# Optimization experiments

Hardware: AMD Instinct MI355X
Metric: run time of the kernel (lower is better)

Reference implementation:

```python
import jax, jax.numpy as jnp
import numpy as np
from jax import lax

B, T, D_IN = 64, 4096, 64
D_EMB, H = 24, 128


def setup_inputs() -> dict:
    key = jax.random.key(0)
    ks = jax.random.split(key, 8)
    s = 0.01  # matches RandomNormal(stddev=0.01) style init
    return {
        "x": jax.random.normal(ks[0], (B, T, D_IN), jnp.float32),
        "W_emb": jax.random.normal(ks[1], (D_IN, D_EMB), jnp.float32) * s,
        "b_emb": jnp.zeros((D_EMB,), jnp.float32),
        "W_f": jax.random.normal(ks[2], (D_EMB + H, H), jnp.float32) * s,
        "b_f": jnp.ones((H,), jnp.float32),  # forget bias init to ones (as in source)
        "W_i": jax.random.normal(ks[3], (D_EMB + H, H), jnp.float32) * s,
        "b_i": jnp.zeros((H,), jnp.float32),
        "W_c": jax.random.normal(ks[4], (D_EMB + H, H), jnp.float32) * s,
        "b_c": jnp.zeros((H,), jnp.float32),
        "W_o": jax.random.normal(ks[5], (D_EMB + H, H), jnp.float32) * s,
        "b_o": jnp.zeros((H,), jnp.float32),
        "W_out": jax.random.normal(ks[6], (H, 1), jnp.float32) * s,
        "b_out": jnp.zeros((1,), jnp.float32),
    }


def reference(x, W_emb, b_emb, W_f, b_f, W_i, b_i, W_c, b_c, W_o, b_o, W_out, b_out):
    # embedding: Dense(24, sigmoid) applied per timestep
    e = jax.nn.sigmoid(jnp.einsum('btd,de->bte', x, W_emb) + b_emb)  # [B,T,24]
    e_t = jnp.swapaxes(e, 0, 1)  # [T,B,24] for scan over time

    def step(carry, et):
        h, c = carry
        z = jnp.concatenate([et, h], axis=-1)            # [B, 24+128]
        f = jax.nn.sigmoid(z @ W_f + b_f)
        i = jax.nn.sigmoid(z @ W_i + b_i)
        g = jnp.tanh(z @ W_c + b_c)
        o = jax.nn.sigmoid(z @ W_o + b_o)
        c_new = c * f + i * g
        h_new = jnp.tanh(c_new) * o
        return (h_new, c_new), None

    h0 = jnp.zeros((x.shape[0], W_f.shape[1]), x.dtype)
    c0 = jnp.zeros_like(h0)
    (hT, _), _ = lax.scan(step, (h0, c0), e_t)
    return jax.nn.sigmoid(hT @ W_out + b_out)  # [B,1]
```

## Files before the change

kernel.cpp:

```cpp
#include <hip/hip_runtime.h>
#include <stdint.h>

namespace {
constexpr int kB = 64, kT = 4096, kDin = 64, kDe = 24, kH = 128;
constexpr int kCh = 16;
constexpr int kNCh = kT / kCh;
constexpr int kRowU = 16;
constexpr int kPS = 20;
constexpr float kLog2e = 1.4426950408889634f;

typedef __attribute__((ext_vector_type(8))) _Float16 frag8;
typedef __attribute__((ext_vector_type(4))) float v4f;
typedef __attribute__((ext_vector_type(8))) int v8i;
union H2U { uint32_t u; _Float16 s[2]; };

__device__ __forceinline__ float rcp_fast(float x){
#if __has_builtin(__builtin_amdgcn_rcpf)
  return __builtin_amdgcn_rcpf(x);
#else
  return 1.0f / x;
#endif
}
__device__ __forceinline__ float exp2_f(float x){
#if __has_builtin(__builtin_amdgcn_exp2f)
  return __builtin_amdgcn_exp2f(x);
#else
  return exp2f(x);
#endif
}
__device__ __forceinline__ float sigmoid_f(float x){
  return rcp_fast(1.0f + __expf(-x));
}
__device__ __forceinline__ uint32_t pack2(float lo, float hi){
  H2U u; u.s[0] = (_Float16)lo; u.s[1] = (_Float16)hi; return u.u;
}
__device__ __forceinline__ uint32_t sw_fp8(float x){
  union{float f; uint32_t u;} v; v.f = x;
  uint32_t s = (v.u >> 24) & 0x80u;
  float a = fabsf(x);
  if (a < 0.0009765625f) return s;
  if (a > 448.0f) a = 448.0f;
  int e; float m = frexpf(a, &e);
  int E = e - 1 + 7;
  uint32_t bits;
  if (E <= 0){
    int q = (int)(a * 512.0f + 0.5f); if (q > 7) q = 7; bits = (uint32_t)q;
  } else {
    int q = (int)(m * 16.0f + 0.5f);
    if (q == 16){ q = 8; ++E; }
    if (E > 15) { E = 15; q = 14; }
    bits = ((uint32_t)E << 3) | ((uint32_t)q & 7u);
  }
  return s | bits;
}
template <bool HI>
__device__ __forceinline__ uint32_t fp8pair(float a, float b, uint32_t old){
#if __has_builtin(__builtin_amdgcn_cvt_pk_fp8_f32)
  return (uint32_t)__builtin_amdgcn_cvt_pk_fp8_f32(a, b, (int)old, HI);
#else
  uint32_t p = sw_fp8(a) | (sw_fp8(b) << 8);
  return HI ? ((old & 0x0000ffffu) | (p << 16)) : ((old & 0xffff0000u) | p);
#endif
}
__device__ __forceinline__ void lgkm_barrier(){
  asm volatile("s_waitcnt lgkmcnt(0)" ::: "memory");
  __builtin_amdgcn_sched_barrier(0);
  __builtin_amdgcn_s_barrier();
  __builtin_amdgcn_sched_barrier(0);
  asm volatile("" ::: "memory");
}
}

__global__ __launch_bounds__(256) void emb_kernel(
    const float* __restrict__ x, const float* __restrict__ W,
    const float* __restrict__ bias, uint32_t* __restrict__ e_out)
{
  int r = blockIdx.x * blockDim.x + threadIdx.x;
  if (r >= kB * kT) return;
  const float4* xr = (const float4*)(x + (size_t)r * kDin);
  float acc[kDe];
#pragma unroll
  for (int k = 0; k < kDe; ++k) acc[k] = bias[k];
#pragma unroll 4
  for (int d4 = 0; d4 < kDin / 4; ++d4){
    float4 xv = xr[d4];
    const float* w0 = W + (size_t)(d4 * 4) * kDe;
#pragma unroll
    for (int k = 0; k < kDe; ++k) acc[k] += xv.x * w0[k];
#pragma unroll
    for (int k = 0; k < kDe; ++k) acc[k] += xv.y * w0[kDe + k];
#pragma unroll
    for (int k = 0; k < kDe; ++k) acc[k] += xv.z * w0[2 * kDe + k];
#pragma unroll
    for (int k = 0; k < kDe; ++k) acc[k] += xv.w * w0[3 * kDe + k];
  }
  uint32_t p[12];
#pragma unroll
  for (int k = 0; k < 12; ++k)
    p[k] = pack2(sigmoid_f(acc[2 * k]), sigmoid_f(acc[2 * k + 1]));
  uint4* dst = (uint4*)(e_out + (size_t)r * kRowU);
  dst[0] = make_uint4(p[0], p[1], p[2],  p[3]);
  dst[1] = make_uint4(p[4], p[5], p[6],  p[7]);
  dst[2] = make_uint4(p[8], p[9], p[10], p[11]);
  dst[3] = make_uint4(0u, 0u, 0u, 0u);
}

__global__ __launch_bounds__(512, 1) void lstm_kernel(
    const uint32_t* __restrict__ e_ws,
    const float* __restrict__ W_f, const float* __restrict__ b_f,
    const float* __restrict__ W_i, const float* __restrict__ b_i,
    const float* __restrict__ W_c, const float* __restrict__ b_c,
    const float* __restrict__ W_o, const float* __restrict__ b_o,
    const float* __restrict__ W_out, const float* __restrict__ b_out,
    float* __restrict__ out)
{
  __shared__ __align__(16) float preh[4 * kH * kPS];
  __shared__ __align__(16) uint32_t elds[kCh * kRowU];
  __shared__ __align__(64) uint32_t hfp8[2 * 32];
  __shared__ float red[8];

  const int b  = blockIdx.x;
  const int t0 = threadIdx.x;
  const int w  = t0 >> 6;
  const int l  = t0 & 63;
  const int q  = l >> 4;
  const int cl = l & 15;
  const int u  = w * 16 + cl;

  const float* Wg[4] = {W_f, W_i, W_c, W_o};
  const float* bgp[4] = {b_f, b_i, b_c, b_o};
  const float scl[4] = {-kLog2e, -kLog2e, -2.0f * kLog2e, -kLog2e};

  v8i B8[4];
#pragma unroll
  for (int g = 0; g < 4; ++g){
    const float sc = scl[g] * 64.0f;
#pragma unroll
    for (int r = 0; r < 8; ++r){
      const float* col = Wg[g] + (size_t)(24 + q * 32 + r * 4) * kH + u;
      uint32_t reg = fp8pair<false>(col[0] * sc, col[kH] * sc, 0u);
      reg = fp8pair<true>(col[2 * kH] * sc, col[3 * kH] * sc, reg);
      B8[g][r] = (int)reg;
    }
  }

  frag8 Bp[4];
  float biasC[4];
#pragma unroll
  for (int g = 0; g < 4; ++g){
    biasC[g] = bgp[g][u] * scl[g];
#pragma unroll
    for (int j = 0; j < 8; ++j){
      int k = q * 8 + j;
      Bp[g][j] = (_Float16)((k < kDe) ? Wg[g][(size_t)k * kH + u] * scl[g] : 0.0f);
    }
  }

  const uint4* e4 = (const uint4*)e_ws;
  const size_t bbase = (size_t)b * kT * 4;

  auto do_pregemm = [&](){
    frag8 Ae = *(const frag8*)&elds[cl * kRowU + q * 4];
#pragma unroll
    for (int g = 0; g < 4; ++g){
      v4f c; c[0] = biasC[g]; c[1] = biasC[g]; c[2] = biasC[g]; c[3] = biasC[g];
      v4f d = __builtin_amdgcn_mfma_f32_16x16x32_f16(Ae, Bp[g], c, 0, 0, 0);
      *(v4f*)&preh[(g * kH + u) * kPS + q * 4] = d;
    }
  };
  float pb[4][kCh];
  auto load_pb = [&](){
#pragma unroll
    for (int g = 0; g < 4; ++g){
      const v4f* src = (const v4f*)&preh[(g * kH + u) * kPS];
#pragma unroll
      for (int r = 0; r < 4; ++r){
        v4f t = src[r];
        pb[g][4*r+0] = t[0]; pb[g][4*r+1] = t[1];
        pb[g][4*r+2] = t[2]; pb[g][4*r+3] = t[3];
      }
    }
  };

  uint4 pre4;
  if (t0 < 64) ((uint4*)elds)[t0] = e4[bbase + t0];
  if (t0 < 32) hfp8[t0] = 0u;
  __syncthreads();
  do_pregemm();
  load_pb();
  if (t0 < 64 && kNCh > 1) pre4 = e4[bbase + (size_t)kCh * 4 + t0];

  float cst = 0.0f, ho = 0.0f;
  const v4f zero4 = {0.0f, 0.0f, 0.0f, 0.0f};

#pragma unroll 1
  for (int cc = 0; cc < kNCh; ++cc){
#pragma unroll
    for (int s = 0; s < kCh; ++s){
      const int cur = (cc * kCh + s) & 1, nxt = cur ^ 1;

      v8i A = *(const v8i*)&hfp8[cur * 32 + q * 8];

      v4f a0 = __builtin_amdgcn_mfma_scale_f32_16x16x128_f8f6f4(
                   A, B8[0], zero4, 0, 0, 0, 121, 0, 121);
      v4f a1 = __builtin_amdgcn_mfma_scale_f32_16x16x128_f8f6f4(
                   A, B8[1], zero4, 0, 0, 0, 121, 0, 121);
      v4f a2 = __builtin_amdgcn_mfma_scale_f32_16x16x128_f8f6f4(
                   A, B8[2], zero4, 0, 0, 0, 121, 0, 121);
      v4f a3 = __builtin_amdgcn_mfma_scale_f32_16x16x128_f8f6f4(
                   A, B8[3], zero4, 0, 0, 0, 121, 0, 121);

      float f  = rcp_fast(1.0f + exp2_f(a0[0] + pb[0][s]));
      float ig = rcp_fast(1.0f + exp2_f(a1[0] + pb[1][s]));
      float g2 = rcp_fast(1.0f + exp2_f(a2[0] + pb[2][s]));
      float og = rcp_fast(1.0f + exp2_f(a3[0] + pb[3][s]));
      float gg = fmaf(g2, 2.0f, -1.0f);
      cst = fmaf(cst, f, ig * gg);
      float rh = rcp_fast(1.0f + exp2_f(-2.0f * kLog2e * cst));
      ho = fmaf(rh, 128.0f, -64.0f) * og;

      if (l < 16){
        uint32_t byte = fp8pair<false>(ho, ho, 0u) & 0xffu;
        ((uint8_t*)&hfp8[nxt * 32])[u] = (uint8_t)byte;
      }
      if (s == kCh - 1 && cc + 1 < kNCh && t0 < 64) ((uint4*)elds)[t0] = pre4;
      lgkm_barrier();
    }

    if (cc + 1 < kNCh){
      do_pregemm();
      load_pb();
      if (t0 < 64 && cc + 2 < kNCh)
        pre4 = e4[bbase + (size_t)(cc + 2) * kCh * 4 + t0];
    }
  }

  float partial = (l < 16) ? ho * (W_out[u] * 0.015625f) : 0.0f;
#pragma unroll
  for (int off = 1; off <= 32; off <<= 1) partial += __shfl_xor(partial, off, 64);
  if (l == 0) red[w] = partial;
  __syncthreads();
  if (t0 == 0){
    float acc = b_out[0];
#pragma unroll
    for (int k = 0; k < 8; ++k) acc += red[k];
    out[b] = sigmoid_f(acc);
  }
}

extern "C" void kernel_launch(void* const* d_in, const int* in_sizes, int n_in,
                              void* d_out, int out_size, void* d_ws, size_t ws_size,
                              hipStream_t stream){
  const float* x     = (const float*)d_in[0];
  const float* W_emb = (const float*)d_in[1];
  const float* b_emb = (const float*)d_in[2];
  const float* W_f   = (const float*)d_in[3];
  const float* b_f   = (const float*)d_in[4];
  const float* W_i   = (const float*)d_in[5];
  const float* b_i   = (const float*)d_in[6];
  const float* W_c   = (const float*)d_in[7];
  const float* b_c   = (const float*)d_in[8];
  const float* W_o   = (const float*)d_in[9];
  const float* b_o   = (const float*)d_in[10];
  const float* W_out = (const float*)d_in[11];
  const float* b_out = (const float*)d_in[12];
  float* out = (float*)d_out;
  uint32_t* e_ws = (uint32_t*)d_ws;

  const int rows = kB * kT;
  emb_kernel<<<(rows + 255) / 256, 256, 0, stream>>>(x, W_emb, b_emb, e_ws);
  lstm_kernel<<<kB, 512, 0, stream>>>(e_ws, W_f, b_f, W_i, b_i, W_c, b_c,
                                      W_o, b_o, W_out, b_out, out);
}
```

Baseline: 1.444 ms.

## Halve LSTM block to 4 waves, each wave handling two hidden-unit slices

Shrinks the recurrent block from 8 to 4 wavefronts, so each wave computes two 16-unit hidden slices per step with 8 MFMAs instead of 4. The goal is cheaper per-step barrier synchronization across fewer waves on the serial time loop. To fit the doubled per-lane state in registers, the precomputed input-projection terms are stored packed as fp16 pairs rather than fp32, which lowers their precision. Per-wave work per step doubles, so the serial critical path may grow.

```diff
diff --git a/kernel.cpp b/kernel.cpp
--- a/kernel.cpp
+++ b/kernel.cpp
@@ -105,7 +105,7 @@
   dst[3] = make_uint4(0u, 0u, 0u, 0u);
 }
 
-__global__ __launch_bounds__(512, 1) void lstm_kernel(
+__global__ __launch_bounds__(256, 1) void lstm_kernel(
     const uint32_t* __restrict__ e_ws,
     const float* __restrict__ W_f, const float* __restrict__ b_f,
     const float* __restrict__ W_i, const float* __restrict__ b_i,
@@ -117,7 +117,7 @@
   __shared__ __align__(16) float preh[4 * kH * kPS];
   __shared__ __align__(16) uint32_t elds[kCh * kRowU];
   __shared__ __align__(64) uint32_t hfp8[2 * 32];
-  __shared__ float red[8];
+  __shared__ float red[4];
 
   const int b  = blockIdx.x;
   const int t0 = threadIdx.x;
@@ -125,34 +125,41 @@
   const int l  = t0 & 63;
   const int q  = l >> 4;
   const int cl = l & 15;
-  const int u  = w * 16 + cl;
+  const int u  = w * 32 + cl;
 
   const float* Wg[4] = {W_f, W_i, W_c, W_o};
   const float* bgp[4] = {b_f, b_i, b_c, b_o};
   const float scl[4] = {-kLog2e, -kLog2e, -2.0f * kLog2e, -kLog2e};
 
-  v8i B8[4];
-#pragma unroll
-  for (int g = 0; g < 4; ++g){
-    const float sc = scl[g] * 64.0f;
-#pragma unroll
-    for (int r = 0; r < 8; ++r){
-      const float* col = Wg[g] + (size_t)(24 + q * 32 + r * 4) * kH + u;
-      uint32_t reg = fp8pair<false>(col[0] * sc, col[kH] * sc, 0u);
-      reg = fp8pair<true>(col[2 * kH] * sc, col[3 * kH] * sc, reg);
-      B8[g][r] = (int)reg;
-    }
-  }
-
-  frag8 Bp[4];
-  float biasC[4];
-#pragma unroll
-  for (int g = 0; g < 4; ++g){
-    biasC[g] = bgp[g][u] * scl[g];
-#pragma unroll
-    for (int j = 0; j < 8; ++j){
-      int k = q * 8 + j;
-      Bp[g][j] = (_Float16)((k < kDe) ? Wg[g][(size_t)k * kH + u] * scl[g] : 0.0f);
+  v8i B8[2][4];
+#pragma unroll
+  for (int sl = 0; sl < 2; ++sl){
+#pragma unroll
+    for (int g = 0; g < 4; ++g){
+      const float sc = scl[g] * 64.0f;
+#pragma unroll
+      for (int r = 0; r < 8; ++r){
+        const float* col = Wg[g] + (size_t)(24 + q * 32 + r * 4) * kH + (u + sl * 16);
+        uint32_t reg = fp8pair<false>(col[0] * sc, col[kH] * sc, 0u);
+        reg = fp8pair<true>(col[2 * kH] * sc, col[3 * kH] * sc, reg);
+        B8[sl][g][r] = (int)reg;
+      }
+    }
+  }
+
+  frag8 Bp[2][4];
+  float biasC[2][4];
+#pragma unroll
+  for (int sl = 0; sl < 2; ++sl){
+#pragma unroll
+    for (int g = 0; g < 4; ++g){
+      biasC[sl][g] = bgp[g][u + sl * 16] * scl[g];
+#pragma unroll
+      for (int j = 0; j < 8; ++j){
+        int k = q * 8 + j;
+        Bp[sl][g][j] =
+            (_Float16)((k < kDe) ? Wg[g][(size_t)k * kH + (u + sl * 16)] * scl[g] : 0.0f);
+      }
     }
   }
 
@@ -162,35 +169,46 @@
   auto do_pregemm = [&](){
     frag8 Ae = *(const frag8*)&elds[cl * kRowU + q * 4];
 #pragma unroll
-    for (int g = 0; g < 4; ++g){
-      v4f c; c[0] = biasC[g]; c[1] = biasC[g]; c[2] = biasC[g]; c[3] = biasC[g];
-      v4f d = __builtin_amdgcn_mfma_f32_16x16x32_f16(Ae, Bp[g], c, 0, 0, 0);
-      *(v4f*)&preh[(g * kH + u) * kPS + q * 4] = d;
+    for (int sl = 0; sl < 2; ++sl){
+#pragma unroll
+      for (int g = 0; g < 4; ++g){
+        v4f c; c[0] = biasC[sl][g]; c[1] = biasC[sl][g];
+        c[2] = biasC[sl][g]; c[3] = biasC[sl][g];
+        v4f d = __builtin_amdgcn_mfma_f32_16x16x32_f16(Ae, Bp[sl][g], c, 0, 0, 0);
+        *(v4f*)&preh[(g * kH + (u + sl * 16)) * kPS + q * 4] = d;
+      }
     }
   };
-  float pb[4][kCh];
+  uint32_t pbp[2][4][kCh / 2];
   auto load_pb = [&](){
 #pragma unroll
-    for (int g = 0; g < 4; ++g){
-      const v4f* src = (const v4f*)&preh[(g * kH + u) * kPS];
-#pragma unroll
-      for (int r = 0; r < 4; ++r){
-        v4f t = src[r];
-        pb[g][4*r+0] = t[0]; pb[g][4*r+1] = t[1];
-        pb[g][4*r+2] = t[2]; pb[g][4*r+3] = t[3];
-      }
-    }
+    for (int sl = 0; sl < 2; ++sl){
+#pragma unroll
+      for (int g = 0; g < 4; ++g){
+        const v4f* src = (const v4f*)&preh[(g * kH + (u + sl * 16)) * kPS];
+#pragma unroll
+        for (int r = 0; r < 4; ++r){
+          v4f t = src[r];
+          pbp[sl][g][2 * r]     = pack2(t[0], t[1]);
+          pbp[sl][g][2 * r + 1] = pack2(t[2], t[3]);
+        }
+      }
+    }
+  };
+  auto upb = [&](int sl, int g, int s) -> float {
+    H2U t; t.u = pbp[sl][g][s >> 1]; return (float)t.s[s & 1];
   };
 
   uint4 pre4;
   if (t0 < 64) ((uint4*)elds)[t0] = e4[bbase + t0];
-  if (t0 < 32) hfp8[t0] = 0u;
+  if (t0 < 64) hfp8[t0] = 0u;
   __syncthreads();
   do_pregemm();
   load_pb();
   if (t0 < 64 && kNCh > 1) pre4 = e4[bbase + (size_t)kCh * 4 + t0];
 
-  float cst = 0.0f, ho = 0.0f;
+  float cst0 = 0.0f, cst1 = 0.0f;
+  float ho0 = 0.0f, ho1 = 0.0f;
   const v4f zero4 = {0.0f, 0.0f, 0.0f, 0.0f};
 
 #pragma unroll 1
@@ -201,27 +219,49 @@
 
       v8i A = *(const v8i*)&hfp8[cur * 32 + q * 8];
 
-      v4f a0 = __builtin_amdgcn_mfma_scale_f32_16x16x128_f8f6f4(
-                   A, B8[0], zero4, 0, 0, 0, 121, 0, 121);
-      v4f a1 = __builtin_amdgcn_mfma_scale_f32_16x16x128_f8f6f4(
-                   A, B8[1], zero4, 0, 0, 0, 121, 0, 121);
-      v4f a2 = __builtin_amdgcn_mfma_scale_f32_16x16x128_f8f6f4(
-                   A, B8[2], zero4, 0, 0, 0, 121, 0, 121);
-      v4f a3 = __builtin_amdgcn_mfma_scale_f32_16x16x128_f8f6f4(
-                   A, B8[3], zero4, 0, 0, 0, 121, 0, 121);
-
-      float f  = rcp_fast(1.0f + exp2_f(a0[0] + pb[0][s]));
-      float ig = rcp_fast(1.0f + exp2_f(a1[0] + pb[1][s]));
-      float g2 = rcp_fast(1.0f + exp2_f(a2[0] + pb[2][s]));
-      float og = rcp_fast(1.0f + exp2_f(a3[0] + pb[3][s]));
-      float gg = fmaf(g2, 2.0f, -1.0f);
-      cst = fmaf(cst, f, ig * gg);
-      float rh = rcp_fast(1.0f + exp2_f(-2.0f * kLog2e * cst));
-      ho = fmaf(rh, 128.0f, -64.0f) * og;
+      v4f a00 = __builtin_amdgcn_mfma_scale_f32_16x16x128_f8f6f4(
+                    A, B8[0][0], zero4, 0, 0, 0, 121, 0, 121);
+      v4f a01 = __builtin_amdgcn_mfma_scale_f32_16x16x128_f8f6f4(
+                    A, B8[0][1], zero4, 0, 0, 0, 121, 0, 121);
+      v4f a02 = __builtin_amdgcn_mfma_scale_f32_16x16x128_f8f6f4(
+                    A, B8[0][2], zero4, 0, 0, 0, 121, 0, 121);
+      v4f a03 = __builtin_amdgcn_mfma_scale_f32_16x16x128_f8f6f4(
+                    A, B8[0][3], zero4, 0, 0, 0, 121, 0, 121);
+      v4f a10 = __builtin_amdgcn_mfma_scale_f32_16x16x128_f8f6f4(
+                    A, B8[1][0], zero4, 0, 0, 0, 121, 0, 121);
+      v4f a11 = __builtin_amdgcn_mfma_scale_f32_16x16x128_f8f6f4(
+                    A, B8[1][1], zero4, 0, 0, 0, 121, 0, 121);
+      v4f a12 = __builtin_amdgcn_mfma_scale_f32_16x16x128_f8f6f4(
+                    A, B8[1][2], zero4, 0, 0, 0, 121, 0, 121);
+      v4f a13 = __builtin_amdgcn_mfma_scale_f32_16x16x128_f8f6f4(
+                    A, B8[1][3], zero4, 0, 0, 0, 121, 0, 121);
+
+      {
+        float f  = rcp_fast(1.0f + exp2_f(a00[0] + upb(0, 0, s)));
+        float ig = rcp_fast(1.0f + exp2_f(a01[0] + upb(0, 1, s)));
+        float g2 = rcp_fast(1.0f + exp2_f(a02[0] + upb(0, 2, s)));
+        float og = rcp_fast(1.0f + exp2_f(a03[0] + upb(0, 3, s)));
+        float gg = fmaf(g2, 2.0f, -1.0f);
+        cst0 = fmaf(cst0, f, ig * gg);
+        float rh = rcp_fast(1.0f + exp2_f(-2.0f * kLog2e * cst0));
+        ho0 = fmaf(rh, 128.0f, -64.0f) * og;
+      }
+      {
+        float f  = rcp_fast(1.0f + exp2_f(a10[0] + upb(1, 0, s)));
+        float ig = rcp_fast(1.0f + exp2_f(a11[0] + upb(1, 1, s)));
+        float g2 = rcp_fast(1.0f + exp2_f(a12[0] + upb(1, 2, s)));
+        float og = rcp_fast(1.0f + exp2_f(a13[0] + upb(1, 3, s)));
+        float gg = fmaf(g2, 2.0f, -1.0f);
+        cst1 = fmaf(cst1, f, ig * gg);
+        float rh = rcp_fast(1.0f + exp2_f(-2.0f * kLog2e * cst1));
+        ho1 = fmaf(rh, 128.0f, -64.0f) * og;
+      }
 
       if (l < 16){
-        uint32_t byte = fp8pair<false>(ho, ho, 0u) & 0xffu;
-        ((uint8_t*)&hfp8[nxt * 32])[u] = (uint8_t)byte;
+        uint32_t pk = fp8pair<false>(ho0, ho1, 0u);
+        uint8_t* hb = (uint8_t*)&hfp8[nxt * 32];
+        hb[u]      = (uint8_t)(pk & 0xffu);
+        hb[u + 16] = (uint8_t)((pk >> 8) & 0xffu);
       }
       if (s == kCh - 1 && cc + 1 < kNCh && t0 < 64) ((uint4*)elds)[t0] = pre4;
       lgkm_barrier();
@@ -235,7 +275,9 @@
     }
   }
 
-  float partial = (l < 16) ? ho * (W_out[u] * 0.015625f) : 0.0f;
+  float partial = 0.0f;
+  if (l < 16)
+    partial = ho0 * (W_out[u] * 0.015625f) + ho1 * (W_out[u + 16] * 0.015625f);
 #pragma unroll
   for (int off = 1; off <= 32; off <<= 1) partial += __shfl_xor(partial, off, 64);
   if (l == 0) red[w] = partial;
@@ -243,7 +285,7 @@
   if (t0 == 0){
     float acc = b_out[0];
 #pragma unroll
-    for (int k = 0; k < 8; ++k) acc += red[k];
+    for (int k = 0; k < 4; ++k) acc += red[k];
     out[b] = sigmoid_f(acc);
   }
 }
@@ -269,6 +311,6 @@
 
   const int rows = kB * kT;
   emb_kernel<<<(rows + 255) / 256, 256, 0, stream>>>(x, W_emb, b_emb, e_ws);
-  lstm_kernel<<<kB, 512, 0, stream>>>(e_ws, W_f, b_f, W_i, b_i, W_c, b_c,
+  lstm_kernel<<<kB, 256, 0, stream>>>(e_ws, W_f, b_f, W_i, b_i, W_c, b_c,
                                       W_o, b_o, W_out, b_out, out);
 }
```

After: 1.861 ms. 1.29x slower.
